# Performance work log

Measured on AMD Instinct MI355X. Metric: run time of the kernel, lower is better.

## Reference

```python
import jax, jax.numpy as jnp
import numpy as np

V, D, B, L = 1_000_000, 128, 16384, 50  # vocab, embed_dim, num_bags, bag_len
N = B * L  # total indices


def setup_inputs() -> dict:
    key = jax.random.key(0)
    k0, k1, k2, k3 = jax.random.split(key, 4)
    # int4-packed table: each byte holds two 4-bit codes (low nibble = even elem)
    weights = jax.random.randint(k0, (V, D // 2), 0, 256, dtype=jnp.int32)
    scales = jax.random.uniform(k1, (V,), jnp.float32, 0.01, 0.1)  # per-row scale
    zeros = jax.random.randint(k2, (V,), 0, 16).astype(jnp.float32)  # per-row zero-point
    indices = jax.random.randint(k3, (N,), 0, V, dtype=jnp.int32)
    offsets = jnp.arange(B + 1, dtype=jnp.int32) * L  # include_last_offset=True
    other_tensor = jax.random.normal(jax.random.fold_in(key, 7), (B, D), jnp.float32)
    return {"weights": weights, "scales": scales, "zeros": zeros,
            "indices": indices, "offsets": offsets, "other_tensor": other_tensor}


def _quant_embedding_bag(weights, scales, zeros, indices, offsets):
    n = indices.shape[0]
    wq = weights[indices]                      # [N, D//2] packed bytes (gather)
    low = wq & 0xF
    high = (wq >> 4) & 0xF
    q = jnp.stack([low, high], axis=-1).reshape(n, D)  # [N, D] int4 codes
    deq = (q.astype(jnp.float32) - zeros[indices][:, None]) * scales[indices][:, None]
    # bag id per index from offsets (include_last_offset -> offsets has B+1 entries)
    seg = jnp.clip(jnp.searchsorted(offsets, jnp.arange(n, dtype=offsets.dtype),
                                    side="right") - 1, 0, B - 1)
    return jax.ops.segment_sum(deq, seg, num_segments=B)  # mode=0 (sum)


def reference(weights, scales, zeros, indices, offsets, other_tensor):
    eb = _quant_embedding_bag(weights, scales, zeros, indices, offsets)
    # eb1 == eb2 (identical calls in the original module); other_tensor_pos=-1, cat_dim=1
    return jnp.concatenate([eb, eb, other_tensor], axis=1)
```

## Files before the change

### kernel.cpp

```cpp
#include <hip/hip_runtime.h>


#define DIM 128

__global__ __launch_bounds__(256) void qebag_kernel(
    const uint4* __restrict__ weights,
    const float* __restrict__ scales,
    const float* __restrict__ zeros,
    const int* __restrict__ indices,
    const int* __restrict__ offsets,
    const float* __restrict__ other,
    float* __restrict__ out,
    int B) {
  const int wave = threadIdx.x >> 6;
  const int lane = threadIdx.x & 63;
  const int g = lane >> 4;
  const int t = lane & 15;
  int bag = blockIdx.x * 4 + wave;
  if (bag >= B) return;
  bag = __builtin_amdgcn_readfirstlane(bag);

  const int start = offsets[bag];
  const int count = offsets[bag + 1] - start;

  const float4* oth4 = (const float4*)(other + (size_t)bag * DIM);
  float4 oth = make_float4(0.f, 0.f, 0.f, 0.f);
  if (lane >= 32) oth = oth4[lane - 32];

  float acc[8];
  #pragma unroll
  for (int k = 0; k < 8; ++k) acc[k] = 0.f;
  float corr = 0.f;

  for (int base = 0; base < count; base += 64) {
    const int cnt = min(64, count - base);

    int idx = 0; float s = 0.f, sz = 0.f;
    if (lane < cnt) {
      idx = indices[start + base + lane];
      s = scales[idx];
      sz = s * zeros[idx];
    }
    float c = sz;
    #pragma unroll
    for (int off = 1; off < 64; off <<= 1) c += __shfl_xor(c, off);
    corr += c;

    int ij[16]; float sj[16];
    #pragma unroll
    for (int i = 0; i < 16; ++i) {
      const int src = 4 * i + g;
      ij[i] = __shfl(idx, src);
      sj[i] = __shfl(s, src);
    }
    uint4 w[16];
    #pragma unroll
    for (int i = 0; i < 16; ++i)
      w[i] = weights[(size_t)(unsigned)ij[i] * 16 + t];
    #pragma unroll
    for (int i = 0; i < 16; ++i) {
      acc[0] = fmaf(sj[i], (float)(w[i].x & 0xFu), acc[0]);
      acc[1] = fmaf(sj[i], (float)((w[i].x >> 4) & 0xFu), acc[1]);
      acc[2] = fmaf(sj[i], (float)(w[i].y & 0xFu), acc[2]);
      acc[3] = fmaf(sj[i], (float)((w[i].y >> 4) & 0xFu), acc[3]);
      acc[4] = fmaf(sj[i], (float)(w[i].z & 0xFu), acc[4]);
      acc[5] = fmaf(sj[i], (float)((w[i].z >> 4) & 0xFu), acc[5]);
      acc[6] = fmaf(sj[i], (float)(w[i].w & 0xFu), acc[6]);
      acc[7] = fmaf(sj[i], (float)((w[i].w >> 4) & 0xFu), acc[7]);
    }
  }

  #pragma unroll
  for (int k = 0; k < 8; ++k) {
    acc[k] += __shfl_xor(acc[k], 16);
    acc[k] += __shfl_xor(acc[k], 32);
    acc[k] -= corr;
  }

  float4* o4 = (float4*)(out + (size_t)bag * (3 * DIM));
  if (g < 2) {
    const float4 lo = make_float4(acc[0], acc[1], acc[2], acc[3]);
    const float4 hi = make_float4(acc[4], acc[5], acc[6], acc[7]);
    o4[g * 32 + 2 * t]     = lo;
    o4[g * 32 + 2 * t + 1] = hi;
  } else {
    o4[64 + (lane - 32)] = oth;
  }
}

extern "C" void kernel_launch(void* const* d_in, const int* in_sizes, int n_in,
                              void* d_out, int out_size, void* d_ws, size_t ws_size,
                              hipStream_t stream) {
  const uint4* weights  = (const uint4*)d_in[0];
  const float* scales   = (const float*)d_in[1];
  const float* zeros    = (const float*)d_in[2];
  const int* indices    = (const int*)d_in[3];
  const int* offsets    = (const int*)d_in[4];
  const float* other    = (const float*)d_in[5];
  float* out            = (float*)d_out;

  const int B = in_sizes[5] / DIM;
  const int blocks = (B + 3) / 4;

  qebag_kernel<<<blocks, 256, 0, stream>>>(weights, scales, zeros, indices,
                                           offsets, other, out, B);
}
```

Before: 349.8 us.

## Repack int32-stored table bytes into dense uint32 rows before gathering

Adds a pre-pass kernel that compresses each row's int32-per-byte storage into packed 32-bit words, shrinking each row from 256 to 64 bytes in a workspace buffer. The bag kernel then gathers the compact rows and unpacks eight nibbles per word. This cuts random gather traffic by a factor of four, but adds a full streaming read of the whole table plus a write of the packed copy on every call.

After: 394.0 us. +12.6%, slower.

```diff
diff --git a/kernel.cpp b/kernel.cpp
--- a/kernel.cpp
+++ b/kernel.cpp
@@ -3,8 +3,19 @@
 
 #define DIM 128
 
+__global__ __launch_bounds__(256) void repack_kernel(
+    const uint4* __restrict__ weights,
+    unsigned* __restrict__ packed,
+    int n) {
+  int i = blockIdx.x * 256 + threadIdx.x;
+  if (i >= n) return;
+  const uint4 w = weights[i];
+  packed[i] = (w.x & 0xFFu) | ((w.y & 0xFFu) << 8) |
+              ((w.z & 0xFFu) << 16) | ((w.w & 0xFFu) << 24);
+}
+
 __global__ __launch_bounds__(256) void qebag_kernel(
-    const uint4* __restrict__ weights,
+    const unsigned* __restrict__ packed,
     const float* __restrict__ scales,
     const float* __restrict__ zeros,
     const int* __restrict__ indices,
@@ -53,20 +64,20 @@
       ij[i] = __shfl(idx, src);
       sj[i] = __shfl(s, src);
     }
-    uint4 w[16];
+    unsigned w[16];
     #pragma unroll
     for (int i = 0; i < 16; ++i)
-      w[i] = weights[(size_t)(unsigned)ij[i] * 16 + t];
+      w[i] = packed[(size_t)(unsigned)ij[i] * 16 + t];
     #pragma unroll
     for (int i = 0; i < 16; ++i) {
-      acc[0] = fmaf(sj[i], (float)(w[i].x & 0xFu), acc[0]);
-      acc[1] = fmaf(sj[i], (float)((w[i].x >> 4) & 0xFu), acc[1]);
-      acc[2] = fmaf(sj[i], (float)(w[i].y & 0xFu), acc[2]);
-      acc[3] = fmaf(sj[i], (float)((w[i].y >> 4) & 0xFu), acc[3]);
-      acc[4] = fmaf(sj[i], (float)(w[i].z & 0xFu), acc[4]);
-      acc[5] = fmaf(sj[i], (float)((w[i].z >> 4) & 0xFu), acc[5]);
-      acc[6] = fmaf(sj[i], (float)(w[i].w & 0xFu), acc[6]);
-      acc[7] = fmaf(sj[i], (float)((w[i].w >> 4) & 0xFu), acc[7]);
+      acc[0] = fmaf(sj[i], (float)(w[i] & 0xFu), acc[0]);
+      acc[1] = fmaf(sj[i], (float)((w[i] >> 4) & 0xFu), acc[1]);
+      acc[2] = fmaf(sj[i], (float)((w[i] >> 8) & 0xFu), acc[2]);
+      acc[3] = fmaf(sj[i], (float)((w[i] >> 12) & 0xFu), acc[3]);
+      acc[4] = fmaf(sj[i], (float)((w[i] >> 16) & 0xFu), acc[4]);
+      acc[5] = fmaf(sj[i], (float)((w[i] >> 20) & 0xFu), acc[5]);
+      acc[6] = fmaf(sj[i], (float)((w[i] >> 24) & 0xFu), acc[6]);
+      acc[7] = fmaf(sj[i], (float)((w[i] >> 28) & 0xFu), acc[7]);
     }
   }
 
@@ -98,10 +109,14 @@
   const int* offsets    = (const int*)d_in[4];
   const float* other    = (const float*)d_in[5];
   float* out            = (float*)d_out;
+  unsigned* packed      = (unsigned*)d_ws;
 
   const int B = in_sizes[5] / DIM;
+  const int npack = in_sizes[0] / 4;
+
+  repack_kernel<<<(npack + 255) / 256, 256, 0, stream>>>(weights, packed, npack);
+
   const int blocks = (B + 3) / 4;
-
-  qebag_kernel<<<blocks, 256, 0, stream>>>(weights, scales, zeros, indices,
+  qebag_kernel<<<blocks, 256, 0, stream>>>(packed, scales, zeros, indices,
                                            offsets, other, out, B);
 }
```
